# Kernel optimization log

Hardware: AMD Instinct MI355X
Metric: run time of the kernel (lower is better)

The kernel has to match this reference:

```python
import jax, jax.numpy as jnp
import numpy as np

BITS = (2, 4, 8)
B, C, H, W = 32, 256, 56, 56
NUM_SEL = 8  # ceil(256 * 3 / 100)


def uniform_quantize(x, bit):
    """Min/max affine uniform quantization to `bit` bits. Returns (dequantized, scale)."""
    qmax = float(2 ** bit - 1)
    mn = jnp.min(x)
    mx = jnp.max(x)
    scale = (mx - mn) / qmax
    q = jnp.clip(jnp.round((x - mn) / scale), 0.0, qmax)
    return q * scale + mn, scale


def setup_inputs() -> dict:
    key = jax.random.key(0)
    k1, k2, k3 = jax.random.split(key, 3)
    inp = jax.random.normal(k1, (B, C, H, W), dtype=jnp.float32)
    beta = jax.random.normal(k2, (len(BITS),), dtype=jnp.float32)
    sel = jax.random.randint(k3, (NUM_SEL,), 0, C, dtype=jnp.int32)
    return {"input": inp, "beta_activ": beta, "selected_channels": sel}


def reference(input, beta_activ, selected_channels):
    sw = jax.nn.softmax(beta_activ, axis=0)          # [n_bits]
    selected = input[:, selected_channels, :, :]      # [B, NUM_SEL, H, W] gather
    activ = jnp.zeros_like(selected)
    scale = jnp.float32(0.0)
    for i, bit in enumerate(BITS):
        out, scale = uniform_quantize(selected, bit)
        activ = activ + out * sw[i]
    # scatter weighted-quantized subset back into a clone of the input
    result = input.at[:, selected_channels, :, :].set(activ)
    return result, scale
```

## Files before the change

### kernel.cpp

```cpp
#include <hip/hip_runtime.h>

#define B_    32
#define C_    256
#define H_    56
#define W_    56
#define HW    (H_ * W_)
#define HW4   (HW / 4)
#define NSEL  8
#define NTOT  (B_ * C_ * HW)
#define NTOT4 (NTOT / 4)
#define NSELTOT4 (B_ * NSEL * HW4)

#define RED_BLOCKS 256
#define TPB        256

typedef float f32x4 __attribute__((ext_vector_type(4)));

__global__ __launch_bounds__(TPB)
void k_minmax(const float* __restrict__ in, const int* __restrict__ sel,
              float* __restrict__ ws) {
    __shared__ float smn[TPB], smx[TPB];
    __shared__ int ssel[NSEL];
    if (threadIdx.x < NSEL) ssel[threadIdx.x] = sel[threadIdx.x];
    __syncthreads();

    float mn = INFINITY, mx = -INFINITY;
    const f32x4* in4 = reinterpret_cast<const f32x4*>(in);
    for (int i = blockIdx.x * TPB + threadIdx.x; i < NSELTOT4;
         i += RED_BLOCKS * TPB) {
        int pos = i % HW4;
        int t   = i / HW4;
        int j   = t % NSEL;
        int b   = t / NSEL;
        f32x4 v = in4[(b * C_ + ssel[j]) * HW4 + pos];
        mn = fminf(mn, fminf(fminf(v.x, v.y), fminf(v.z, v.w)));
        mx = fmaxf(mx, fmaxf(fmaxf(v.x, v.y), fmaxf(v.z, v.w)));
    }
    smn[threadIdx.x] = mn;
    smx[threadIdx.x] = mx;
    __syncthreads();
    for (int s = TPB / 2; s > 0; s >>= 1) {
        if (threadIdx.x < s) {
            smn[threadIdx.x] = fminf(smn[threadIdx.x], smn[threadIdx.x + s]);
            smx[threadIdx.x] = fmaxf(smx[threadIdx.x], smx[threadIdx.x + s]);
        }
        __syncthreads();
    }
    if (threadIdx.x == 0) {
        ws[blockIdx.x]              = smn[0];
        ws[RED_BLOCKS + blockIdx.x] = smx[0];
    }
}

__device__ __forceinline__ float qmix(float x, float mn,
                                      float sc2, float sc4, float sc8,
                                      float sw0, float sw1, float sw2) {
    float d = x - mn;
    float q2 = fminf(fmaxf(rintf(d / sc2), 0.0f), 3.0f);
    float q4 = fminf(fmaxf(rintf(d / sc4), 0.0f), 15.0f);
    float q8 = fminf(fmaxf(rintf(d / sc8), 0.0f), 255.0f);
    float o2 = q2 * sc2 + mn;
    float o4 = q4 * sc4 + mn;
    float o8 = q8 * sc8 + mn;
    return o2 * sw0 + o4 * sw1 + o8 * sw2;
}

__global__ __launch_bounds__(TPB)
void k_main2(const float* __restrict__ in, const float* __restrict__ beta,
             const int* __restrict__ sel, float* __restrict__ out,
             const float* __restrict__ ws) {
    __shared__ float smn[TPB], smx[TPB];
    __shared__ int flags[C_];
    const int tid = threadIdx.x;

    smn[tid] = ws[tid];
    smx[tid] = ws[RED_BLOCKS + tid];
    __syncthreads();
    for (int s = TPB / 2; s > 0; s >>= 1) {
        if (tid < s) {
            smn[tid] = fminf(smn[tid], smn[tid + s]);
            smx[tid] = fmaxf(smx[tid], smx[tid + s]);
        }
        __syncthreads();
    }
    const float mnf = smn[0];
    const float mxf = smx[0];

    int f = 0;
    #pragma unroll
    for (int j = 0; j < NSEL; ++j) f |= (sel[j] == tid) ? 1 : 0;
    flags[tid] = f;
    __syncthreads();

    const float b0 = beta[0], b1 = beta[1], b2 = beta[2];
    const float bm = fmaxf(b0, fmaxf(b1, b2));
    const float e0 = expf(b0 - bm), e1 = expf(b1 - bm), e2 = expf(b2 - bm);
    const float inv = 1.0f / (e0 + e1 + e2);
    const float sw0 = e0 * inv, sw1 = e1 * inv, sw2 = e2 * inv;

    const float range = mxf - mnf;
    const float sc2 = range / 3.0f;
    const float sc4 = range / 15.0f;
    const float sc8 = range / 255.0f;

    if (blockIdx.x == 0 && tid == 0) out[NTOT] = sc8;

    const f32x4* in4 = reinterpret_cast<const f32x4*>(in);
    f32x4* out4 = reinterpret_cast<f32x4*>(out);
    for (int i = blockIdx.x * TPB + tid; i < NTOT4;
         i += gridDim.x * TPB) {
        f32x4 v = in4[i];
        int c = (i / HW4) % C_;
        if (flags[c]) {
            v.x = qmix(v.x, mnf, sc2, sc4, sc8, sw0, sw1, sw2);
            v.y = qmix(v.y, mnf, sc2, sc4, sc8, sw0, sw1, sw2);
            v.z = qmix(v.z, mnf, sc2, sc4, sc8, sw0, sw1, sw2);
            v.w = qmix(v.w, mnf, sc2, sc4, sc8, sw0, sw1, sw2);
        }
        out4[i] = v;
    }
}

extern "C" void kernel_launch(void* const* d_in, const int* in_sizes, int n_in,
                              void* d_out, int out_size, void* d_ws, size_t ws_size,
                              hipStream_t stream) {
    const float* input = (const float*)d_in[0];
    const float* beta  = (const float*)d_in[1];
    const int*   sel   = (const int*)d_in[2];
    float* out = (float*)d_out;
    float* ws  = (float*)d_ws;

    k_minmax<<<RED_BLOCKS, TPB, 0, stream>>>(input, sel, ws);
    k_main2<<<4096, TPB, 0, stream>>>(input, beta, sel, out, ws);
}
```

Measured before the change: 193.2 us.

## Map one block per channel plane and cut reduction prologue overhead

The main copy kernel now launches one block per (batch, channel) plane. Each block loads the plane with four unrolled vector loads and a per-block selected-channel flag, so the per-element channel divide/modulo and the grid-stride loop go away. The final min/max reduction is done with a single-wavefront shuffle over 64 partials, and the constants are broadcast through shared memory, replacing the 256-entry tree reduction that every block repeated. The first-pass reduction grid shrinks from 256 to 64 blocks, which gives that kernel less parallelism over the selected channels.

```diff
diff --git a/kernel.cpp b/kernel.cpp
--- a/kernel.cpp
+++ b/kernel.cpp
@@ -2,17 +2,16 @@
 
 #define B_    32
 #define C_    256
-#define H_    56
-#define W_    56
-#define HW    (H_ * W_)
-#define HW4   (HW / 4)
+#define HW    3136
+#define HW4   784
 #define NSEL  8
 #define NTOT  (B_ * C_ * HW)
 #define NTOT4 (NTOT / 4)
 #define NSELTOT4 (B_ * NSEL * HW4)
+#define PLANES (B_ * C_)
 
-#define RED_BLOCKS 256
-#define TPB        256
+#define RB  64
+#define TPB 256
 
 typedef float f32x4 __attribute__((ext_vector_type(4)));
 
@@ -27,7 +26,7 @@
     float mn = INFINITY, mx = -INFINITY;
     const f32x4* in4 = reinterpret_cast<const f32x4*>(in);
     for (int i = blockIdx.x * TPB + threadIdx.x; i < NSELTOT4;
-         i += RED_BLOCKS * TPB) {
+         i += RB * TPB) {
         int pos = i % HW4;
         int t   = i / HW4;
         int j   = t % NSEL;
@@ -47,8 +46,8 @@
         __syncthreads();
     }
     if (threadIdx.x == 0) {
-        ws[blockIdx.x]              = smn[0];
-        ws[RED_BLOCKS + blockIdx.x] = smx[0];
+        ws[blockIdx.x]      = smn[0];
+        ws[RB + blockIdx.x] = smx[0];
     }
 }
 
@@ -65,60 +64,79 @@
     return o2 * sw0 + o4 * sw1 + o8 * sw2;
 }
 
+__device__ __forceinline__ void qmix4(f32x4& v, float mn,
+                                      float sc2, float sc4, float sc8,
+                                      float sw0, float sw1, float sw2) {
+    v.x = qmix(v.x, mn, sc2, sc4, sc8, sw0, sw1, sw2);
+    v.y = qmix(v.y, mn, sc2, sc4, sc8, sw0, sw1, sw2);
+    v.z = qmix(v.z, mn, sc2, sc4, sc8, sw0, sw1, sw2);
+    v.w = qmix(v.w, mn, sc2, sc4, sc8, sw0, sw1, sw2);
+}
+
 __global__ __launch_bounds__(TPB)
-void k_main2(const float* __restrict__ in, const float* __restrict__ beta,
+void k_main3(const float* __restrict__ in, const float* __restrict__ beta,
              const int* __restrict__ sel, float* __restrict__ out,
              const float* __restrict__ ws) {
-    __shared__ float smn[TPB], smx[TPB];
-    __shared__ int flags[C_];
+    __shared__ float cns[8];
     const int tid = threadIdx.x;
 
-    smn[tid] = ws[tid];
-    smx[tid] = ws[RED_BLOCKS + tid];
+    if (tid < 64) {
+        float pm = ws[tid];
+        float px = ws[RB + tid];
+        #pragma unroll
+        for (int o = 32; o > 0; o >>= 1) {
+            pm = fminf(pm, __shfl_down(pm, o));
+            px = fmaxf(px, __shfl_down(px, o));
+        }
+        if (tid == 0) {
+            const float mnf = pm, mxf = px;
+            const float b0 = beta[0], b1 = beta[1], b2 = beta[2];
+            const float bm = fmaxf(b0, fmaxf(b1, b2));
+            const float e0 = expf(b0 - bm), e1 = expf(b1 - bm),
+                        e2 = expf(b2 - bm);
+            const float inv = 1.0f / (e0 + e1 + e2);
+            const float range = mxf - mnf;
+            cns[0] = mnf;
+            cns[1] = range / 3.0f;
+            cns[2] = range / 15.0f;
+            cns[3] = range / 255.0f;
+            cns[4] = e0 * inv;
+            cns[5] = e1 * inv;
+            cns[6] = e2 * inv;
+            if (blockIdx.x == 0) out[NTOT] = range / 255.0f;
+        }
+    }
     __syncthreads();
-    for (int s = TPB / 2; s > 0; s >>= 1) {
-        if (tid < s) {
-            smn[tid] = fminf(smn[tid], smn[tid + s]);
-            smx[tid] = fmaxf(smx[tid], smx[tid + s]);
-        }
-        __syncthreads();
+    const float mnf = cns[0], sc2 = cns[1], sc4 = cns[2], sc8 = cns[3];
+    const float sw0 = cns[4], sw1 = cns[5], sw2 = cns[6];
+
+    const int plane = blockIdx.x;
+    const int c = plane & (C_ - 1);
+    bool f = false;
+    #pragma unroll
+    for (int j = 0; j < NSEL; ++j) f = f || (sel[j] == c);
+
+    const f32x4* __restrict__ src =
+        reinterpret_cast<const f32x4*>(in) + (size_t)plane * HW4;
+    f32x4* __restrict__ dst =
+        reinterpret_cast<f32x4*>(out) + (size_t)plane * HW4;
+
+    f32x4 v0 = src[tid];
+    f32x4 v1 = src[tid + 256];
+    f32x4 v2 = src[tid + 512];
+    f32x4 v3 = src[(tid < 16) ? (tid + 768) : (HW4 - 1)];
+
+    if (f) {
+        qmix4(v0, mnf, sc2, sc4, sc8, sw0, sw1, sw2);
+        qmix4(v1, mnf, sc2, sc4, sc8, sw0, sw1, sw2);
+        qmix4(v2, mnf, sc2, sc4, sc8, sw0, sw1, sw2);
+        qmix4(v3, mnf, sc2, sc4, sc8, sw0, sw1, sw2);
     }
-    const float mnf = smn[0];
-    const float mxf = smx[0];
 
-    int f = 0;
-    #pragma unroll
-    for (int j = 0; j < NSEL; ++j) f |= (sel[j] == tid) ? 1 : 0;
-    flags[tid] = f;
-    __syncthreads();
-
-    const float b0 = beta[0], b1 = beta[1], b2 = beta[2];
-    const float bm = fmaxf(b0, fmaxf(b1, b2));
-    const float e0 = expf(b0 - bm), e1 = expf(b1 - bm), e2 = expf(b2 - bm);
-    const float inv = 1.0f / (e0 + e1 + e2);
-    const float sw0 = e0 * inv, sw1 = e1 * inv, sw2 = e2 * inv;
-
-    const float range = mxf - mnf;
-    const float sc2 = range / 3.0f;
-    const float sc4 = range / 15.0f;
-    const float sc8 = range / 255.0f;
-
-    if (blockIdx.x == 0 && tid == 0) out[NTOT] = sc8;
-
-    const f32x4* in4 = reinterpret_cast<const f32x4*>(in);
-    f32x4* out4 = reinterpret_cast<f32x4*>(out);
-    for (int i = blockIdx.x * TPB + tid; i < NTOT4;
-         i += gridDim.x * TPB) {
-        f32x4 v = in4[i];
-        int c = (i / HW4) % C_;
-        if (flags[c]) {
-            v.x = qmix(v.x, mnf, sc2, sc4, sc8, sw0, sw1, sw2);
-            v.y = qmix(v.y, mnf, sc2, sc4, sc8, sw0, sw1, sw2);
-            v.z = qmix(v.z, mnf, sc2, sc4, sc8, sw0, sw1, sw2);
-            v.w = qmix(v.w, mnf, sc2, sc4, sc8, sw0, sw1, sw2);
-        }
-        out4[i] = v;
-    }
+    dst[tid]       = v0;
+    dst[tid + 256] = v1;
+    dst[tid + 512] = v2;
+    if (tid < 16) dst[tid + 768] = v3;
 }
 
 extern "C" void kernel_launch(void* const* d_in, const int* in_sizes, int n_in,
@@ -130,6 +148,6 @@
     float* out = (float*)d_out;
     float* ws  = (float*)d_ws;
 
-    k_minmax<<<RED_BLOCKS, TPB, 0, stream>>>(input, sel, ws);
-    k_main2<<<4096, TPB, 0, stream>>>(input, beta, sel, out, ws);
+    k_minmax<<<RB, TPB, 0, stream>>>(input, sel, ws);
+    k_main3<<<PLANES, TPB, 0, stream>>>(input, beta, sel, out, ws);
 }
```

After: 196.9 us. About the same (+1.9%).
